# Performance work log

Hardware: AMD Instinct MI355X
Metric: run time of the kernel (lower is better)

## Reference

```python
import math
import jax, jax.numpy as jnp
import numpy as np

T = 1000
MAX_BETA = 0.2
B = 65536
NUM_CLASSES = np.array([2,2,3,4,5,6,8,10,10,12,16,16,20,24,32,40,2,3,4,5,6,8,10,50])
F_CAT = len(NUM_CLASSES)            # 24 categorical features
D_CAT = int(NUM_CLASSES.sum())      # 298 total one-hot columns
NUM_NUM = 16                        # numerical features
OFF = np.concatenate([[0], np.cumsum(NUM_CLASSES)])

# cosine schedule, exactly as get_named_beta_schedule('cosine', T, max_beta=0.2)
def _cosine_betas(n, max_beta):
    ab = lambda u: math.cos((u + 0.008) / 1.008 * math.pi / 2) ** 2
    return np.array([min(1.0 - ab((i + 1) / n) / ab(i / n), max_beta) for i in range(n)])

_betas = _cosine_betas(T, MAX_BETA)
_la = np.log(1.0 - _betas)           # log alpha_t (float64)
_lca = np.cumsum(_la)                # log alpha_bar_t
LOG_ALPHA = jnp.asarray(_la.astype(np.float32))
LOG_1M_ALPHA = jnp.asarray(np.log(-np.expm1(_la)).astype(np.float32))
LOG_CA = jnp.asarray(_lca.astype(np.float32))
LOG_1M_CA = jnp.asarray(np.log(-np.expm1(_lca)).astype(np.float32))
SEG = jnp.asarray(np.repeat(np.arange(F_CAT), NUM_CLASSES))          # [D_CAT] feature id per column
LOG_K = jnp.asarray(np.log(np.repeat(NUM_CLASSES, NUM_CLASSES).astype(np.float64)).astype(np.float32))
OFF_J = jnp.asarray(OFF[:-1])


def log_add_exp(a, b):
    m = jnp.maximum(a, b)
    return m + jnp.log(jnp.exp(a - m) + jnp.exp(b - m))


def sliced_logsumexp(x):
    # ragged per-feature logsumexp over variable-width class slices; x: [B, D_CAT]
    xt = x.T                                                     # [D_CAT, B]
    m = jax.ops.segment_max(xt, SEG, num_segments=F_CAT)         # [F_CAT, B]
    s = jax.ops.segment_sum(jnp.exp(xt - m[SEG]), SEG, num_segments=F_CAT)
    return (m + jnp.log(s))[SEG].T                               # [B, D_CAT]


def sliced_max(x):
    xt = x.T
    m = jax.ops.segment_max(xt, SEG, num_segments=F_CAT)
    return m[SEG].T


def q_pred(log_x, t):
    # log q(x_t | x_0): log_add_exp(log_x + log a_bar_t, log(1 - a_bar_t) - log K)
    return log_add_exp(log_x + LOG_CA[t][:, None], LOG_1M_CA[t][:, None] - LOG_K)


def q_pred_one_timestep(log_x_t, t):
    return log_add_exp(log_x_t + LOG_ALPHA[t][:, None], LOG_1M_ALPHA[t][:, None] - LOG_K)


def q_posterior(log_x0, log_x_t, t):
    tm1 = jnp.maximum(t - 1, 0)
    lev = q_pred(log_x0, tm1)
    lev = jnp.where((t == 0)[:, None], log_x0, lev)              # t==0 -> delta on x_0
    un = lev + q_pred_one_timestep(log_x_t, t)
    return un - sliced_logsumexp(un)


def _forward(x_cat_idx, t, noise, u_cat, model_out):
    b = x_cat_idx.shape[0]
    # index_to_log_onehot over ragged slices
    cols = OFF_J[None, :] + x_cat_idx                            # [B, F_CAT]
    oh = jnp.zeros((b, D_CAT), jnp.float32).at[jnp.arange(b)[:, None], cols].set(1.0)
    log_x_start = jnp.log(jnp.clip(oh, 1e-30))
    # multinomial q_sample via per-feature gumbel-argmax
    log_ev = q_pred(log_x_start, t)
    gumbel = -jnp.log(-jnp.log(jnp.clip(u_cat, 1e-30, 1.0)))
    scores = log_ev + gumbel
    sample_oh = (scores >= sliced_max(scores)).astype(jnp.float32)
    log_x_t = jnp.log(jnp.clip(sample_oh, 1e-30))
    # split denoiser output
    model_out_num = model_out[:, :NUM_NUM]
    model_out_cat = model_out[:, NUM_NUM:]
    # p_pred: ragged log-softmax of logits then posterior
    log_x0_recon = model_out_cat - sliced_logsumexp(model_out_cat)
    log_model_prob = q_posterior(log_x0_recon, log_x_t, t)
    log_true_prob = q_posterior(log_x_start, log_x_t, t)
    kl = jnp.sum(jnp.exp(log_true_prob) * (log_true_prob - log_model_prob), axis=1)
    decoder_nll = -jnp.sum(jnp.exp(log_x_start) * log_model_prob, axis=1)
    lt = jnp.where(t == 0, decoder_nll, kl)
    # prior KL against uniform over each feature's classes
    qxT = q_pred(log_x_start, jnp.full_like(t, T - 1))
    kl_prior = jnp.sum(jnp.exp(qxT) * (qxT + LOG_K), axis=1)
    loss_multi = (lt * T + kl_prior) / F_CAT                     # pt = 1/T uniform sampling
    # gaussian mse loss (gaussian_loss_type='mse', eps parametrization)
    loss_gauss = jnp.mean((noise - model_out_num) ** 2, axis=1)
    return loss_multi + loss_gauss                               # [B]


def setup_inputs() -> dict:
    key = jax.random.key(0)
    k1, k2, k3, k4, k5 = jax.random.split(key, 5)
    x_cat_idx = jax.random.randint(k1, (B, F_CAT), 0, jnp.asarray(NUM_CLASSES))
    t = jax.random.randint(k2, (B,), 0, T)
    noise = jax.random.normal(k3, (B, NUM_NUM), jnp.float32)
    u_cat = jax.random.uniform(k4, (B, D_CAT), jnp.float32)
    model_out = jax.random.normal(k5, (B, NUM_NUM + D_CAT), jnp.float32)
    return {"x_cat_idx": x_cat_idx, "t": t, "noise": noise, "u_cat": u_cat, "model_out": model_out}


def reference(x_cat_idx, t, noise, u_cat, model_out):
    return _forward(x_cat_idx, t, noise, u_cat, model_out)
```

## Files before the change

kernel.cpp:

```cpp
#include <hip/hip_runtime.h>
#include <math.h>

#define T_STEPS 1000
#define B_ROWS 65536
#define N_FCAT 24
#define N_DCAT 298
#define NUM_NUM 16
#define MO_STRIDE 314
#define NKID 14
#define NEGL -69.07755278982137f
#define NINF -1e38f

__constant__ int c_numc[N_FCAT] = {2,2,3,4,5,6,8,10,10,12,16,16,20,24,32,40,2,3,4,5,6,8,10,50};
__constant__ int c_kval[NKID]   = {2,3,4,5,6,8,10,12,16,20,24,32,40,50};

__constant__ int c1K[6][2]   = {{8,6},{6,5},{5,4},{4,3},{3,2},{2,2}};
__constant__ int c1OFF[6][2] = {{230,16},{224,11},{219,7},{215,4},{212,0},{210,2}};
__constant__ int c1KID[6][2] = {{5,4},{4,3},{3,2},{2,1},{1,0},{0,0}};
__constant__ int c1F[6][2]   = {{21,5},{20,4},{19,3},{18,2},{17,0},{16,1}};

__constant__ int c2K[3][2]   = {{16,12},{10,10},{10,8}};
__constant__ int c2OFF[3][2] = {{78,50},{30,40},{238,22}};
__constant__ int c2KID[3][2] = {{8,7},{6,6},{6,5}};
__constant__ int c2F[3][2]   = {{11,9},{7,8},{22,6}};

__constant__ int c4K[2][2]   = {{32,24},{20,16}};
__constant__ int c4OFF[2][2] = {{138,114},{94,62}};
__constant__ int c4KID[2][2] = {{11,10},{9,8}};
__constant__ int c4F[2][2]   = {{14,13},{12,10}};

__device__ float  g_sched[4*T_STEPS];
__device__ float  g_ecap[T_STEPS];
__device__ float4 g_tab4[T_STEPS*NKID*3];
__device__ float  g_klp;

__device__ __forceinline__ float lae(float a, float b) {
  float m = fmaxf(a, b);
  return m + logf(expf(a - m) + expf(b - m));
}
__device__ __forceinline__ double lad(double a, double b) {
  double m = fmax(a, b);
  return m + log(exp(a - m) + exp(b - m));
}

__global__ void build_sched_kernel() {
  __shared__ double sh[1024];
  int i = threadIdx.x;
  double la = 0.0;
  if (i < T_STEPS) {
    const double PI = 3.14159265358979323846;
    double u0 = (double)i / 1000.0, u1 = (double)(i + 1) / 1000.0;
    double c0 = cos((u0 + 0.008) / 1.008 * PI * 0.5);
    double c1 = cos((u1 + 0.008) / 1.008 * PI * 0.5);
    double beta = 1.0 - (c1 * c1) / (c0 * c0);
    if (beta > 0.2) beta = 0.2;
    la = log(1.0 - beta);
  }
  sh[i] = la;
  __syncthreads();
  double run = la;
  for (int ofs = 1; ofs < 1024; ofs <<= 1) {
    double add = (i >= ofs) ? sh[i - ofs] : 0.0;
    __syncthreads();
    run += add;
    sh[i] = run;
    __syncthreads();
  }
  if (i < T_STEPS) {
    g_sched[i]               = (float)la;
    g_sched[T_STEPS + i]     = (float)log(-expm1(la));
    g_sched[2 * T_STEPS + i] = (float)run;
    g_sched[3 * T_STEPS + i] = (float)log(-expm1(run));
  }
}

__global__ void build_tab_kernel() {
  int e = blockIdx.x * blockDim.x + threadIdx.x;
  if (e < T_STEPS * NKID) {
    int t = e / NKID, k = e - t * NKID;
    bool t0 = (t == 0);
    int tm1 = t0 ? 0 : t - 1;
    float la = g_sched[t], l1a = g_sched[T_STEPS + t];
    float lca = g_sched[2 * T_STEPS + t], l1ca = g_sched[3 * T_STEPS + t];
    float lca_p = g_sched[2 * T_STEPS + tm1], l1ca_p = g_sched[3 * T_STEPS + tm1];
    float logK = (float)log((double)c_kval[k]);
    float cb_t = l1ca - logK;
    float ev_h = lae(lca, cb_t);
    float ev_n = lae(NEGL + lca, cb_t);
    double cb1 = (double)l1a - (double)logK;
    double q1h = lad((double)la, cb1);
    double q1n = lad((double)NEGL + (double)la, cb1);
    double cbp = (double)l1ca_p - (double)logK;
    double levth = t0 ? 0.0 : lad((double)lca_p, cbp);
    double levtn = t0 ? (double)NEGL : lad((double)NEGL + (double)lca_p, cbp);
    float4* o = g_tab4 + e * 3;
    o[0] = make_float4(ev_h, ev_n, (float)q1h, (float)q1n);
    o[1] = make_float4((float)exp(q1h), (float)exp(q1n), (float)exp(levth), (float)exp(levtn));
    o[2] = make_float4((float)levth, (float)levtn, t0 ? 0.f : (float)exp(cbp), 0.f);
    if (k == 0) g_ecap[t] = t0 ? 1.f : (float)exp((double)lca_p);
  }
  if (e == 0) {
    double lcaT = g_sched[2 * T_STEPS + T_STEPS - 1];
    double l1caT = g_sched[3 * T_STEPS + T_STEPS - 1];
    double s = 0.0;
    for (int f = 0; f < N_FCAT; ++f) {
      double logK = log((double)c_numc[f]);
      double cbT = l1caT - logK;
      double qh = lad(lcaT, cbT);
      double qn = lad((double)NEGL + lcaT, cbT);
      s += exp(qh) * (qh + logK) + (double)(c_numc[f] - 1) * exp(qn) * (qn + logK);
    }
    g_klp = (float)s;
  }
}

__device__ __forceinline__ float osum(float v) {
  v += __int_as_float(__builtin_amdgcn_mov_dpp(__float_as_int(v), 0xB1, 0xF, 0xF, true));
  v += __int_as_float(__builtin_amdgcn_mov_dpp(__float_as_int(v), 0x4E, 0xF, 0xF, true));
  v += __int_as_float(__builtin_amdgcn_mov_dpp(__float_as_int(v), 0x141, 0xF, 0xF, true));
  return v;
}
__device__ __forceinline__ void oargmax(float& smax, int& jm) {
  float os; int oj;
  os = __int_as_float(__builtin_amdgcn_mov_dpp(__float_as_int(smax), 0xB1, 0xF, 0xF, true));
  oj = __builtin_amdgcn_mov_dpp(jm, 0xB1, 0xF, 0xF, true);
  if (os > smax || (os == smax && oj < jm)) { smax = os; jm = oj; }
  os = __int_as_float(__builtin_amdgcn_mov_dpp(__float_as_int(smax), 0x4E, 0xF, 0xF, true));
  oj = __builtin_amdgcn_mov_dpp(jm, 0x4E, 0xF, 0xF, true);
  if (os > smax || (os == smax && oj < jm)) { smax = os; jm = oj; }
  os = __int_as_float(__builtin_amdgcn_mov_dpp(__float_as_int(smax), 0x141, 0xF, 0xF, true));
  oj = __builtin_amdgcn_mov_dpp(jm, 0x141, 0xF, 0xF, true);
  if (os > smax || (os == smax && oj < jm)) { smax = os; jm = oj; }
}
__device__ __forceinline__ float mirror16_add(float v) {
  return v + __int_as_float(__builtin_amdgcn_mov_dpp(__float_as_int(v), 0x140, 0xF, 0xF, true));
}

template <int NJ>
__device__ __forceinline__ float pair_body(int g, int K, int off, int h, bool t0, float ecap,
                                           const float* __restrict__ mocat,
                                           const float* __restrict__ urow,
                                           const float4* __restrict__ tb)
{
  float4 ta = tb[0], tbv = tb[1], tc = tb[2];
  float ev_h = ta.x, ev_n = ta.y, q1h = ta.z, q1n = ta.w;
  float q1he = tbv.x, q1ne = tbv.y, eth = tbv.z, etn = tbv.w;
  float levth = tc.x, levtn = tc.y, cbpe = tc.z;

  float xv[NJ];
  #pragma unroll
  for (int jj = 0; jj < NJ; ++jj) {
    int j = jj * 8 + g;
    int jc = (j < K) ? j : (K - 1);
    xv[jj] = mocat[off + jc];
  }

  float s1 = 0.f, smax = NINF;
  int jm = 0x7fffffff;
  #pragma unroll
  for (int jj = 0; jj < NJ; ++jj) {
    int j = jj * 8 + g;
    int jc = (j < K) ? j : (K - 1);
    bool in = (j < K);
    float e = __expf(xv[jj]);
    xv[jj] = e;
    s1 += in ? e : 0.f;
    float u = urow[off + jc];
    u = fminf(fmaxf(u, 1e-30f), 1.0f);
    float gum = -logf(-logf(u));
    float sc = ((j == h) ? ev_h : ev_n) + gum;
    if (in && sc > smax) { smax = sc; jm = j; }
  }
  s1 = osum(s1);
  oargmax(smax, jm);

  float ca = ecap * __builtin_amdgcn_rcpf(s1);

  float Sm = 0.f, Bv = 0.f, lmh = 0.f;
  #pragma unroll
  for (int jj = 0; jj < NJ; ++jj) {
    int j = jj * 8 + g;
    bool in = (j < K);
    float E = fmaf(xv[jj], ca, cbpe);
    float lm = __logf(E);
    float qe = (j == jm) ? q1he : q1ne;
    Sm = in ? fmaf(E, qe, Sm) : Sm;
    float c = ((j == h) ? eth : etn) * qe;
    Bv = in ? fmaf(c, lm, Bv) : Bv;
    lmh += (in && j == h) ? lm : 0.f;
  }
  Sm = osum(Sm); Bv = osum(Bv); lmh = osum(lmh);

  float lse_m = __logf(Sm);
  bool hm = (h == jm);
  float Kf2 = (float)K - 2.f + (hm ? 1.f : 0.f);
  float coefH = eth * (hm ? q1he : q1ne);
  float coefJ = hm ? 0.f : etn * q1he;
  float cn = etn * q1ne;
  float A  = cn * levtn * Kf2 + coefH * levth + coefJ * levtn;
  float St = cn * Kf2 + coefH + coefJ;
  float kl = (A - Bv) * __builtin_amdgcn_rcpf(St) - __logf(St) + lse_m;
  float unh = lmh + (hm ? q1h : q1n);
  float dec = lse_m - unh;
  return t0 ? dec : kl;
}

__device__ __forceinline__ float big_feat(int g, int K, int off, int h, bool t0, float ecap,
                                          const float* __restrict__ mocat,
                                          const float* __restrict__ urow,
                                          const float4* __restrict__ tb)
{
  float4 ta = tb[0], tbv = tb[1], tc = tb[2];
  float ev_h = ta.x, ev_n = ta.y, q1h = ta.z, q1n = ta.w;
  float q1he = tbv.x, q1ne = tbv.y, eth = tbv.z, etn = tbv.w;
  float levth = tc.x, levtn = tc.y, cbpe = tc.z;

  float s1 = 0.f, smax = NINF;
  int jm = 0x7fffffff;
  #pragma unroll 1
  for (int j = g; j < K; j += 8) {
    float x = mocat[off + j];
    s1 += __expf(x);
    float u = urow[off + j];
    u = fminf(fmaxf(u, 1e-30f), 1.0f);
    float gum = -logf(-logf(u));
    float sc = ((j == h) ? ev_h : ev_n) + gum;
    if (sc > smax) { smax = sc; jm = j; }
  }
  s1 = osum(s1);
  oargmax(smax, jm);

  float ca = ecap * __builtin_amdgcn_rcpf(s1);

  float Sm = 0.f, Bv = 0.f, lmh = 0.f;
  #pragma unroll 1
  for (int j = g; j < K; j += 8) {
    float E = fmaf(__expf(mocat[off + j]), ca, cbpe);
    float lm = __logf(E);
    float qe = (j == jm) ? q1he : q1ne;
    Sm = fmaf(E, qe, Sm);
    float c = ((j == h) ? eth : etn) * qe;
    Bv = fmaf(c, lm, Bv);
    lmh += (j == h) ? lm : 0.f;
  }
  Sm = osum(Sm); Bv = osum(Bv); lmh = osum(lmh);

  float lse_m = __logf(Sm);
  bool hm = (h == jm);
  float Kf2 = (float)K - 2.f + (hm ? 1.f : 0.f);
  float coefH = eth * (hm ? q1he : q1ne);
  float coefJ = hm ? 0.f : etn * q1he;
  float cn = etn * q1ne;
  float A  = cn * levtn * Kf2 + coefH * levth + coefJ * levtn;
  float St = cn * Kf2 + coefH + coefJ;
  float kl = (A - Bv) * __builtin_amdgcn_rcpf(St) - __logf(St) + lse_m;
  float unh = lmh + (hm ? q1h : q1n);
  float dec = lse_m - unh;
  return t0 ? dec : kl;
}

__global__ __launch_bounds__(256) void gmd_kernel(
    const int* __restrict__ xci, const int* __restrict__ tarr,
    const float* __restrict__ noise, const float* __restrict__ ucat,
    const float* __restrict__ mo, float* __restrict__ out)
{
  int tid = blockIdx.x * blockDim.x + threadIdx.x;
  int row    = tid >> 4;
  int lane16 = tid & 15;
  int g      = tid & 7;
  int sel    = (lane16 >> 3);
  if (row >= B_ROWS) return;

  int t = tarr[row];
  bool t0 = (t == 0);
  float ecap = g_ecap[t];
  const float4* tabt = g_tab4 + (size_t)t * NKID * 3;
  const int* xrow = xci + (size_t)row * N_FCAT;

  const float* morow = mo + (size_t)row * MO_STRIDE;
  const float* mocat = morow + NUM_NUM;
  const float* urow  = ucat + (size_t)row * N_DCAT;

  float gauss;
  {
    float d = noise[row * NUM_NUM + lane16] - morow[lane16];
    gauss = d * d;
  }

  float multi = 0.f;
  #pragma unroll 1
  for (int p = 0; p < 6; ++p)
    multi += pair_body<1>(g, c1K[p][sel], c1OFF[p][sel], xrow[c1F[p][sel]],
                          t0, ecap, mocat, urow, tabt + c1KID[p][sel] * 3);
  #pragma unroll 1
  for (int p = 0; p < 3; ++p)
    multi += pair_body<2>(g, c2K[p][sel], c2OFF[p][sel], xrow[c2F[p][sel]],
                          t0, ecap, mocat, urow, tabt + c2KID[p][sel] * 3);
  #pragma unroll 1
  for (int p = 0; p < 2; ++p)
    multi += pair_body<4>(g, c4K[p][sel], c4OFF[p][sel], xrow[c4F[p][sel]],
                          t0, ecap, mocat, urow, tabt + c4KID[p][sel] * 3);
  multi += big_feat(g, sel ? 40 : 50, sel ? 170 : 248, xrow[sel ? 15 : 23],
                    t0, ecap, mocat, urow, tabt + (sel ? 12 : 13) * 3);

  multi = mirror16_add(multi);
  gauss = osum(gauss);
  gauss = mirror16_add(gauss);

  if (lane16 == 0) out[row] = (multi * 1000.f + g_klp) / 24.f + gauss / 16.f;
}

extern "C" void kernel_launch(void* const* d_in, const int* in_sizes, int n_in,
                              void* d_out, int out_size, void* d_ws, size_t ws_size,
                              hipStream_t stream) {
  const int*   xci   = (const int*)d_in[0];
  const int*   tarr  = (const int*)d_in[1];
  const float* noise = (const float*)d_in[2];
  const float* ucat  = (const float*)d_in[3];
  const float* mo    = (const float*)d_in[4];
  float* out = (float*)d_out;
  (void)d_ws; (void)ws_size;

  hipLaunchKernelGGL(build_sched_kernel, dim3(1), dim3(1024), 0, stream);
  hipLaunchKernelGGL(build_tab_kernel, dim3((T_STEPS * NKID + 255) / 256), dim3(256), 0, stream);
  hipLaunchKernelGGL(gmd_kernel, dim3((B_ROWS * 16) / 256), dim3(256), 0, stream,
                     xci, tarr, noise, ucat, mo, out);
}
```

Before: 122.1 us.

## Process small categorical features in 4-lane quads to cut idle lanes

Regroups the per-row feature work so that small-K features (K≤10) are handled by 4-lane groups, four features at once per 16-lane row team, instead of 8-lane groups handling two features. This aims to reduce lanes left idle on tiny class slices and the number of serial feature iterations. A new quad reduction with a half-mirror DPP combine is added, and the remaining larger features stay on the 8-lane path. The quad body also caches exponentials in registers to avoid reloading model outputs.

After: 108.9 us. 10.7% less time.

```diff
diff --git a/kernel.cpp b/kernel.cpp
--- a/kernel.cpp
+++ b/kernel.cpp
@@ -14,20 +14,20 @@
 __constant__ int c_numc[N_FCAT] = {2,2,3,4,5,6,8,10,10,12,16,16,20,24,32,40,2,3,4,5,6,8,10,50};
 __constant__ int c_kval[NKID]   = {2,3,4,5,6,8,10,12,16,20,24,32,40,50};
 
-__constant__ int c1K[6][2]   = {{8,6},{6,5},{5,4},{4,3},{3,2},{2,2}};
-__constant__ int c1OFF[6][2] = {{230,16},{224,11},{219,7},{215,4},{212,0},{210,2}};
-__constant__ int c1KID[6][2] = {{5,4},{4,3},{3,2},{2,1},{1,0},{0,0}};
-__constant__ int c1F[6][2]   = {{21,5},{20,4},{19,3},{18,2},{17,0},{16,1}};
-
-__constant__ int c2K[3][2]   = {{16,12},{10,10},{10,8}};
-__constant__ int c2OFF[3][2] = {{78,50},{30,40},{238,22}};
-__constant__ int c2KID[3][2] = {{8,7},{6,6},{6,5}};
-__constant__ int c2F[3][2]   = {{11,9},{7,8},{22,6}};
-
-__constant__ int c4K[2][2]   = {{32,24},{20,16}};
-__constant__ int c4OFF[2][2] = {{138,114},{94,62}};
-__constant__ int c4KID[2][2] = {{11,10},{9,8}};
-__constant__ int c4F[2][2]   = {{14,13},{12,10}};
+__constant__ int p4K[2][2]   = {{32,24},{20,16}};
+__constant__ int p4OFF[2][2] = {{138,114},{94,62}};
+__constant__ int p4KID[2][2] = {{11,10},{9,8}};
+__constant__ int p4F[2][2]   = {{14,13},{12,10}};
+
+__constant__ int qAK[4]   = {10,10,10,8};
+__constant__ int qAOFF[4] = {30,40,238,22};
+__constant__ int qAKID[4] = {6,6,6,5};
+__constant__ int qAF[4]   = {7,8,22,6};
+
+__constant__ int q2K[3][4]   = {{8,6,6,5},{5,4,4,3},{3,2,2,2}};
+__constant__ int q2OFF[3][4] = {{230,16,224,11},{219,7,215,4},{212,0,2,210}};
+__constant__ int q2KID[3][4] = {{5,4,4,3},{3,2,2,1},{1,0,0,0}};
+__constant__ int q2F[3][4]   = {{21,5,20,4},{19,3,18,2},{17,0,1,16}};
 
 __device__ float  g_sched[4*T_STEPS];
 __device__ float  g_ecap[T_STEPS];
@@ -132,8 +132,25 @@
   oj = __builtin_amdgcn_mov_dpp(jm, 0x141, 0xF, 0xF, true);
   if (os > smax || (os == smax && oj < jm)) { smax = os; jm = oj; }
 }
+__device__ __forceinline__ float qsum4(float v) {
+  v += __int_as_float(__builtin_amdgcn_mov_dpp(__float_as_int(v), 0xB1, 0xF, 0xF, true));
+  v += __int_as_float(__builtin_amdgcn_mov_dpp(__float_as_int(v), 0x4E, 0xF, 0xF, true));
+  return v;
+}
+__device__ __forceinline__ void qargmax4(float& smax, int& jm) {
+  float os; int oj;
+  os = __int_as_float(__builtin_amdgcn_mov_dpp(__float_as_int(smax), 0xB1, 0xF, 0xF, true));
+  oj = __builtin_amdgcn_mov_dpp(jm, 0xB1, 0xF, 0xF, true);
+  if (os > smax || (os == smax && oj < jm)) { smax = os; jm = oj; }
+  os = __int_as_float(__builtin_amdgcn_mov_dpp(__float_as_int(smax), 0x4E, 0xF, 0xF, true));
+  oj = __builtin_amdgcn_mov_dpp(jm, 0x4E, 0xF, 0xF, true);
+  if (os > smax || (os == smax && oj < jm)) { smax = os; jm = oj; }
+}
 __device__ __forceinline__ float mirror16_add(float v) {
   return v + __int_as_float(__builtin_amdgcn_mov_dpp(__float_as_int(v), 0x140, 0xF, 0xF, true));
+}
+__device__ __forceinline__ float halfmirror_add(float v) {
+  return v + __int_as_float(__builtin_amdgcn_mov_dpp(__float_as_int(v), 0x141, 0xF, 0xF, true));
 }
 
 template <int NJ>
@@ -205,45 +222,60 @@
   return t0 ? dec : kl;
 }
 
-__device__ __forceinline__ float big_feat(int g, int K, int off, int h, bool t0, float ecap,
-                                          const float* __restrict__ mocat,
-                                          const float* __restrict__ urow,
-                                          const float4* __restrict__ tb)
+template <int NJ>
+__device__ __forceinline__ float quad_body(int g4, int K, int off, int h, bool t0, float ecap,
+                                           const float* __restrict__ mocat,
+                                           const float* __restrict__ urow,
+                                           const float4* __restrict__ tb)
 {
   float4 ta = tb[0], tbv = tb[1], tc = tb[2];
   float ev_h = ta.x, ev_n = ta.y, q1h = ta.z, q1n = ta.w;
   float q1he = tbv.x, q1ne = tbv.y, eth = tbv.z, etn = tbv.w;
   float levth = tc.x, levtn = tc.y, cbpe = tc.z;
 
+  float xv[NJ];
+  #pragma unroll
+  for (int jj = 0; jj < NJ; ++jj) {
+    int j = jj * 4 + g4;
+    int jc = (j < K) ? j : (K - 1);
+    xv[jj] = mocat[off + jc];
+  }
+
   float s1 = 0.f, smax = NINF;
   int jm = 0x7fffffff;
-  #pragma unroll 1
-  for (int j = g; j < K; j += 8) {
-    float x = mocat[off + j];
-    s1 += __expf(x);
-    float u = urow[off + j];
+  #pragma unroll
+  for (int jj = 0; jj < NJ; ++jj) {
+    int j = jj * 4 + g4;
+    int jc = (j < K) ? j : (K - 1);
+    bool in = (j < K);
+    float e = __expf(xv[jj]);
+    xv[jj] = e;
+    s1 += in ? e : 0.f;
+    float u = urow[off + jc];
     u = fminf(fmaxf(u, 1e-30f), 1.0f);
     float gum = -logf(-logf(u));
     float sc = ((j == h) ? ev_h : ev_n) + gum;
-    if (sc > smax) { smax = sc; jm = j; }
-  }
-  s1 = osum(s1);
-  oargmax(smax, jm);
+    if (in && sc > smax) { smax = sc; jm = j; }
+  }
+  s1 = qsum4(s1);
+  qargmax4(smax, jm);
 
   float ca = ecap * __builtin_amdgcn_rcpf(s1);
 
   float Sm = 0.f, Bv = 0.f, lmh = 0.f;
-  #pragma unroll 1
-  for (int j = g; j < K; j += 8) {
-    float E = fmaf(__expf(mocat[off + j]), ca, cbpe);
+  #pragma unroll
+  for (int jj = 0; jj < NJ; ++jj) {
+    int j = jj * 4 + g4;
+    bool in = (j < K);
+    float E = fmaf(xv[jj], ca, cbpe);
     float lm = __logf(E);
     float qe = (j == jm) ? q1he : q1ne;
-    Sm = fmaf(E, qe, Sm);
+    Sm = in ? fmaf(E, qe, Sm) : Sm;
     float c = ((j == h) ? eth : etn) * qe;
-    Bv = fmaf(c, lm, Bv);
-    lmh += (j == h) ? lm : 0.f;
-  }
-  Sm = osum(Sm); Bv = osum(Bv); lmh = osum(lmh);
+    Bv = in ? fmaf(c, lm, Bv) : Bv;
+    lmh += (in && j == h) ? lm : 0.f;
+  }
+  Sm = qsum4(Sm); Bv = qsum4(Bv); lmh = qsum4(lmh);
 
   float lse_m = __logf(Sm);
   bool hm = (h == jm);
@@ -259,6 +291,60 @@
   return t0 ? dec : kl;
 }
 
+__device__ __forceinline__ float big_feat(int g, int K, int off, int h, bool t0, float ecap,
+                                          const float* __restrict__ mocat,
+                                          const float* __restrict__ urow,
+                                          const float4* __restrict__ tb)
+{
+  float4 ta = tb[0], tbv = tb[1], tc = tb[2];
+  float ev_h = ta.x, ev_n = ta.y, q1h = ta.z, q1n = ta.w;
+  float q1he = tbv.x, q1ne = tbv.y, eth = tbv.z, etn = tbv.w;
+  float levth = tc.x, levtn = tc.y, cbpe = tc.z;
+
+  float s1 = 0.f, smax = NINF;
+  int jm = 0x7fffffff;
+  #pragma unroll 1
+  for (int j = g; j < K; j += 8) {
+    float x = mocat[off + j];
+    s1 += __expf(x);
+    float u = urow[off + j];
+    u = fminf(fmaxf(u, 1e-30f), 1.0f);
+    float gum = -logf(-logf(u));
+    float sc = ((j == h) ? ev_h : ev_n) + gum;
+    if (sc > smax) { smax = sc; jm = j; }
+  }
+  s1 = osum(s1);
+  oargmax(smax, jm);
+
+  float ca = ecap * __builtin_amdgcn_rcpf(s1);
+
+  float Sm = 0.f, Bv = 0.f, lmh = 0.f;
+  #pragma unroll 1
+  for (int j = g; j < K; j += 8) {
+    float E = fmaf(__expf(mocat[off + j]), ca, cbpe);
+    float lm = __logf(E);
+    float qe = (j == jm) ? q1he : q1ne;
+    Sm = fmaf(E, qe, Sm);
+    float c = ((j == h) ? eth : etn) * qe;
+    Bv = fmaf(c, lm, Bv);
+    lmh += (j == h) ? lm : 0.f;
+  }
+  Sm = osum(Sm); Bv = osum(Bv); lmh = osum(lmh);
+
+  float lse_m = __logf(Sm);
+  bool hm = (h == jm);
+  float Kf2 = (float)K - 2.f + (hm ? 1.f : 0.f);
+  float coefH = eth * (hm ? q1he : q1ne);
+  float coefJ = hm ? 0.f : etn * q1he;
+  float cn = etn * q1ne;
+  float A  = cn * levtn * Kf2 + coefH * levth + coefJ * levtn;
+  float St = cn * Kf2 + coefH + coefJ;
+  float kl = (A - Bv) * __builtin_amdgcn_rcpf(St) - __logf(St) + lse_m;
+  float unh = lmh + (hm ? q1h : q1n);
+  float dec = lse_m - unh;
+  return t0 ? dec : kl;
+}
+
 __global__ __launch_bounds__(256) void gmd_kernel(
     const int* __restrict__ xci, const int* __restrict__ tarr,
     const float* __restrict__ noise, const float* __restrict__ ucat,
@@ -268,7 +354,9 @@
   int row    = tid >> 4;
   int lane16 = tid & 15;
   int g      = tid & 7;
+  int g4     = tid & 3;
   int sel    = (lane16 >> 3);
+  int qsel   = (lane16 >> 2);
   if (row >= B_ROWS) return;
 
   int t = tarr[row];
@@ -287,23 +375,29 @@
     gauss = d * d;
   }
 
-  float multi = 0.f;
+  float multi8 = 0.f;
   #pragma unroll 1
-  for (int p = 0; p < 6; ++p)
-    multi += pair_body<1>(g, c1K[p][sel], c1OFF[p][sel], xrow[c1F[p][sel]],
-                          t0, ecap, mocat, urow, tabt + c1KID[p][sel] * 3);
+  for (int p = 0; p < 2; ++p)
+    multi8 += pair_body<4>(g, p4K[p][sel], p4OFF[p][sel], xrow[p4F[p][sel]],
+                           t0, ecap, mocat, urow, tabt + p4KID[p][sel] * 3);
+  multi8 += pair_body<2>(g, sel ? 12 : 16, sel ? 50 : 78, xrow[sel ? 9 : 11],
+                         t0, ecap, mocat, urow, tabt + (sel ? 7 : 8) * 3);
+  multi8 += big_feat(g, sel ? 40 : 50, sel ? 170 : 248, xrow[sel ? 15 : 23],
+                     t0, ecap, mocat, urow, tabt + (sel ? 12 : 13) * 3);
+
+  float multi4 = 0.f;
+  multi4 += quad_body<3>(g4, qAK[qsel], qAOFF[qsel], xrow[qAF[qsel]],
+                         t0, ecap, mocat, urow, tabt + qAKID[qsel] * 3);
   #pragma unroll 1
   for (int p = 0; p < 3; ++p)
-    multi += pair_body<2>(g, c2K[p][sel], c2OFF[p][sel], xrow[c2F[p][sel]],
-                          t0, ecap, mocat, urow, tabt + c2KID[p][sel] * 3);
-  #pragma unroll 1
-  for (int p = 0; p < 2; ++p)
-    multi += pair_body<4>(g, c4K[p][sel], c4OFF[p][sel], xrow[c4F[p][sel]],
-                          t0, ecap, mocat, urow, tabt + c4KID[p][sel] * 3);
-  multi += big_feat(g, sel ? 40 : 50, sel ? 170 : 248, xrow[sel ? 15 : 23],
-                    t0, ecap, mocat, urow, tabt + (sel ? 12 : 13) * 3);
-
-  multi = mirror16_add(multi);
+    multi4 += quad_body<2>(g4, q2K[p][qsel], q2OFF[p][qsel], xrow[q2F[p][qsel]],
+                           t0, ecap, mocat, urow, tabt + q2KID[p][qsel] * 3);
+
+  multi8 = mirror16_add(multi8);
+  multi4 = halfmirror_add(multi4);
+  multi4 = mirror16_add(multi4);
+  float multi = multi8 + multi4;
+
   gauss = osum(gauss);
   gauss = mirror16_add(gauss);
 
```
